# Kernel optimization log

Hardware: AMD Instinct MI355X
Metric: run time of the kernel (lower is better)

## Reference

```python
import jax, jax.numpy as jnp
import numpy as np

B, N, M, E, H, A = 2048, 768, 8192, 512, 8, 64  # batch, n, m, embed_dim, heads, head_dim(a)


def setup_inputs() -> dict:
    key = jax.random.key(0)
    ks = jax.random.split(key, 16)
    s = 0.02
    return {
        "x": jax.random.normal(ks[0], (B, N), jnp.float32),
        "X_cross": jax.random.normal(ks[1], (M, N), jnp.float32),
        # manual projection weights (used as x @ W, i.e. nn.Linear .weight of shape [out,in] -> here stored [n, E] etc.)
        "W_q_w": jax.random.normal(ks[2], (N, E), jnp.float32) * s,
        "W_k_w": jax.random.normal(ks[3], (N, E), jnp.float32) * s,
        "W_v_w": jax.random.normal(ks[4], (N, N), jnp.float32) * s,
        # nn.MultiheadAttention internal projections (vdim=n -> separate q/k/v weights)
        "q_w": jax.random.normal(ks[5], (E, E), jnp.float32) * s,
        "k_w": jax.random.normal(ks[6], (E, E), jnp.float32) * s,
        "v_w": jax.random.normal(ks[7], (E, N), jnp.float32) * s,
        "b_q": jax.random.normal(ks[8], (E,), jnp.float32) * s,
        "b_k": jax.random.normal(ks[9], (E,), jnp.float32) * s,
        "b_v": jax.random.normal(ks[10], (E,), jnp.float32) * s,
        "out_w": jax.random.normal(ks[11], (E, E), jnp.float32) * s,
        "out_b": jax.random.normal(ks[12], (E,), jnp.float32) * s,
        # final W_o: nn.Linear(E, n)
        "W_o_w": jax.random.normal(ks[13], (N, E), jnp.float32) * s,
        "W_o_b": jax.random.normal(ks[14], (N,), jnp.float32) * s,
    }


def reference(x, X_cross, W_q_w, W_k_w, W_v_w, q_w, k_w, v_w, b_q, b_k, b_v, out_w, out_b, W_o_w, W_o_b):
    inv_sqrt_a = jnp.float32(1.0 / np.sqrt(A))
    # manual projections (note: the F.layer_norm loop in the source is a no-op)
    Q = (x @ W_q_w) * inv_sqrt_a           # [B, E]; extra 1/sqrt(a) scaling applied pre-MHA
    K = X_cross @ W_k_w                    # [m, E]
    V = X_cross @ W_v_w                    # [m, n]
    # nn.MultiheadAttention (unbatched 2D inputs -> seq lens B and m)
    q = (Q @ q_w.T + b_q).reshape(B, H, A)
    k = (K @ k_w.T + b_k).reshape(M, H, A)
    v = (V @ v_w.T + b_v).reshape(M, H, A)
    scores = jnp.einsum('bha,mha->hbm', q, k) * inv_sqrt_a  # MHA's own 1/sqrt(head_dim)
    attn = jax.nn.softmax(scores, axis=-1)                  # [H, B, m]
    f = attn.mean(axis=0)                                   # averaged attn weights [B, m]
    ctx = jnp.einsum('hbm,mha->bha', attn, v).reshape(B, E)
    attn_out = ctx @ out_w.T + out_b                        # MHA out_proj -> [B, E]
    x_hat = attn_out @ W_o_w.T + W_o_b                      # [B, n]
    return (x, x_hat, f, V)
```

## Files before the change

### kernel.cpp

```cpp
#include <hip/hip_runtime.h>
#include <hip/hip_bf16.h>

typedef unsigned short u16;
typedef unsigned int u32;
typedef __attribute__((ext_vector_type(8))) __bf16 bf16x8;
typedef __attribute__((ext_vector_type(4))) float f32x4;

#define Bd  2048
#define Nd  768
#define Md  8192
#define Ed  512
#define Hd  8
#define NSL 8
#define AIT 16

__device__ __forceinline__ u16 f2bf(float f){
    union { __bf16 b; u16 u; } c; c.b = (__bf16)f; return c.u;
}
__device__ __forceinline__ float bf2f(u16 u){
    union { unsigned u; float f; } a; a.u = ((unsigned)u)<<16; return a.f;
}
__device__ __forceinline__ u32 pack2(float a, float b){
    union { ushort2 s; u32 u; } r;
    r.s.x = f2bf(a); r.s.y = f2bf(b);
    return r.u;
}
__device__ __forceinline__ float fexp2(float x){ return __builtin_amdgcn_exp2f(x); }

__device__ __forceinline__ void glds16(const void* g, void* l){
    __builtin_amdgcn_global_load_lds((const __attribute__((address_space(1))) void*)g,
                                     (__attribute__((address_space(3))) void*)l, 16, 0, 0);
}

struct CvtSeg { const float* src; u16* dst; float* dstf; int n4; };
struct PrepArgs {
    CvtSeg s[9]; int total4;
    const float* Wv; u16* WvT;
    const float* ow; u16* owT;
    const float* Wo; const float* ob; const float* Wob; float* bo;
    float* sume;
};
#define PREP_CVT_BLKS 10320
#define TCVT0_BLKS 576
#define TCVT1_BLKS 256
#define GEMV_BLKS 192
#define ZERO_BLKS 16

__global__ __launch_bounds__(256, 8)
void prep_k(PrepArgs a){
    __shared__ float t[32][33];
    const int bid = blockIdx.x, tid = threadIdx.x;
    if (bid < PREP_CVT_BLKS){
        int i = bid*256 + tid;
        if (i >= a.total4) return;
        #pragma unroll
        for (int k=0;k<9;k++){
            if (i < a.s[k].n4){
                float4 v = *(const float4*)(a.s[k].src + (size_t)i*4);
                if (a.s[k].dstf) *(float4*)(a.s[k].dstf + (size_t)i*4) = v;
                ushort4 u; u.x=f2bf(v.x); u.y=f2bf(v.y); u.z=f2bf(v.z); u.w=f2bf(v.w);
                *(ushort4*)(a.s[k].dst + (size_t)i*4) = u;
                return;
            }
            i -= a.s[k].n4;
        }
        return;
    }
    int local = bid - PREP_CVT_BLKS;
    if (local < TCVT0_BLKS + TCVT1_BLKS){
        const float* in; u16* out; int R, bx, by;
        if (local < TCVT0_BLKS){ in=a.Wv; out=a.WvT; R=Nd; bx=local%24; by=local/24; }
        else { int l2=local-TCVT0_BLKS; in=a.ow; out=a.owT; R=Ed; bx=l2%16; by=l2/16; }
        const int tx = tid & 31, ty = tid >> 5;
        const int r0 = by*32, c0 = bx*32;
        #pragma unroll
        for (int i=0;i<4;i++)
            t[ty + i*8][tx] = in[(size_t)(r0+ty+i*8)*R + c0+tx];
        __syncthreads();
        #pragma unroll
        for (int i=0;i<4;i++)
            out[(size_t)(c0+ty+i*8)*R + r0+tx] = f2bf(t[tx][ty+i*8]);
        return;
    }
    local -= TCVT0_BLKS + TCVT1_BLKS;
    if (local < GEMV_BLKS){
        const int wave = tid >> 6, lane = tid & 63;
        const int i = local*4 + wave;
        float s = 0.f;
        for (int j = lane; j < 512; j += 64) s += a.Wo[(size_t)i*512 + j] * a.ob[j];
        #pragma unroll
        for (int off = 32; off; off >>= 1) s += __shfl_down(s, off);
        if (lane == 0) a.bo[i] = s + a.Wob[i];
        return;
    }
    local -= GEMV_BLKS;
    {
        int idx = local*1024 + tid*4;
        *(float4*)(a.sume + idx) = make_float4(0.f,0.f,0.f,0.f);
    }
}

struct GSeg {
    const u16* A; const u16* B; void* C; const float* bias;
    int M, N, K; float alpha, bscale; int biasmode, outf32, blk0, nbx;
};
struct GBatch { GSeg s[5]; int nseg; };

__global__ __launch_bounds__(256, 3)
void gemm_multi(GBatch gb)
{
    __shared__ u16 lA[128*64];
    __shared__ u16 lB[128*64];
    const int bid = blockIdx.x;
    int si = 0;
    #pragma unroll
    for (int k=1;k<5;k++) if (k < gb.nseg && bid >= gb.s[k].blk0) si = k;
    const GSeg sg = gb.s[si];
    const int local = bid - sg.blk0;
    const int bx = local % sg.nbx, by = local / sg.nbx;
    const int K = sg.K, N = sg.N;

    const int tid = threadIdx.x;
    const int wave = tid >> 6, lane = tid & 63;
    const int wr = wave >> 1, wc = wave & 1;
    const size_t row0 = (size_t)by * 128;
    const size_t col0 = (size_t)bx * 128;

    f32x4 acc[4][4] = {};

    const int srow = wave*32 + (lane>>3);
    const int scol = (lane&7)*8;
    const u16* gA = sg.A + (row0 + srow)*(size_t)K + scol;
    const u16* gB = sg.B + (col0 + srow)*(size_t)K + scol;

    for (int kt = 0; kt < K; kt += 64) {
        #pragma unroll
        for (int i = 0; i < 4; ++i) {
            glds16(gA + (size_t)i*8*K + kt, lA + (wave*32 + i*8)*64);
            glds16(gB + (size_t)i*8*K + kt, lB + (wave*32 + i*8)*64);
        }
        __syncthreads();
        #pragma unroll
        for (int ks = 0; ks < 2; ++ks) {
            bf16x8 af[4], bfv[4];
            #pragma unroll
            for (int i = 0; i < 4; ++i)
                af[i] = *(const bf16x8*)&lA[(wr*64 + i*16 + (lane&15))*64 + ks*32 + (lane>>4)*8];
            #pragma unroll
            for (int i = 0; i < 4; ++i)
                bfv[i] = *(const bf16x8*)&lB[(wc*64 + i*16 + (lane&15))*64 + ks*32 + (lane>>4)*8];
            #pragma unroll
            for (int mi = 0; mi < 4; ++mi)
                #pragma unroll
                for (int ni = 0; ni < 4; ++ni)
                    acc[mi][ni] = __builtin_amdgcn_mfma_f32_16x16x32_bf16(af[mi], bfv[ni], acc[mi][ni], 0, 0, 0);
        }
        __syncthreads();
    }

    #pragma unroll
    for (int mi = 0; mi < 4; ++mi) {
        #pragma unroll
        for (int j = 0; j < 4; ++j) {
            const size_t r = row0 + wr*64 + mi*16 + (lane>>4)*4 + j;
            float badd_r = (sg.biasmode==2) ? sg.bias[r]*sg.bscale : 0.f;
            #pragma unroll
            for (int ni = 0; ni < 4; ++ni) {
                const size_t c = col0 + wc*64 + ni*16 + (lane&15);
                float bv = (sg.biasmode==1) ? sg.bias[c]*sg.bscale : badd_r;
                float v = acc[mi][ni][j] * sg.alpha + bv;
                if (sg.outf32) ((float*)sg.C)[r*(size_t)N + c] = v;
                else           ((u16*)sg.C)[r*(size_t)N + c] = f2bf(v);
            }
        }
    }
}

__global__ __launch_bounds__(256, 2)
void attn_sc(const u16* __restrict__ qp, const u16* __restrict__ kp,
             const u16* __restrict__ vTp, float* __restrict__ sumexp,
             u16* __restrict__ part)
{
    __shared__ u16 lK[2][64*64];
    __shared__ u16 lV[2][64*64];
    __shared__ u16 lP[4][64*64];
    const int tid = threadIdx.x, w = tid>>6, l = tid&63;
    const int g = l>>4, b15 = l&15;
    const int h = blockIdx.x & 7;
    const int rest = blockIdx.x >> 3;
    const int msl = rest & (NSL-1), bt = rest >> 3;
    const int m0 = msl * (AIT*64);

    bf16x8 qf[4][2];
    #pragma unroll
    for (int rt=0; rt<4; ++rt)
        #pragma unroll
        for (int ks=0; ks<2; ++ks)
            qf[rt][ks] = *(const bf16x8*)&qp[(size_t)(bt*256 + w*64 + rt*16 + b15)*512
                                            + h*64 + ks*32 + g*8];

    int addrW[4][4], addrR[4][2];
    #pragma unroll
    for (int rt=0; rt<4; ++rt){
        int bl = rt*16 + b15;
        #pragma unroll
        for (int ct=0; ct<4; ++ct){
            int chunk = ct*2 + (g>>1);
            addrW[rt][ct] = bl*128 + ((chunk ^ (bl&7))<<4) + (g&1)*8;
        }
        #pragma unroll
        for (int ks2=0; ks2<2; ++ks2)
            addrR[rt][ks2] = bl*128 + (((ks2*4+g) ^ (bl&7))<<4);
    }

    const int srcc = ((l&7) ^ (l>>3))*8;
    char* lPw = (char*)lP[w];

    auto STAGE = [&](int buf, int mb){
        #pragma unroll
        for (int i=0;i<2;i++)
            glds16(kp + (size_t)(mb + w*16 + i*8 + (l>>3))*512 + h*64 + srcc,
                   &lK[buf][(w*16 + i*8)*64]);
        #pragma unroll
        for (int i=0;i<2;i++)
            glds16(vTp + (size_t)(h*64 + w*16 + i*8 + (l>>3))*8192 + mb + srcc,
                   &lV[buf][(w*16 + i*8)*64]);
    };

    STAGE(0, m0);
    __syncthreads();

    f32x4 cacc[4][4] = {};
    float rs[4] = {};
    int cur = 0;
    for (int t=0; t<AIT; ++t){
        if (t+1 < AIT) STAGE(cur^1, m0 + (t+1)*64);

        f32x4 sacc[4][4] = {};
        #pragma unroll
        for (int ks=0; ks<2; ++ks){
            bf16x8 bk[4];
            #pragma unroll
            for (int ct=0; ct<4; ++ct)
                bk[ct] = *(const bf16x8*)&lK[cur][(ct*16+b15)*64 + (((ks*4+g) ^ (b15&7))<<3)];
            #pragma unroll
            for (int rt=0; rt<4; ++rt)
                #pragma unroll
                for (int ct=0; ct<4; ++ct)
                    sacc[rt][ct] = __builtin_amdgcn_mfma_f32_16x16x32_bf16(bk[ct], qf[rt][ks], sacc[rt][ct],0,0,0);
        }
        #pragma unroll
        for (int rt=0; rt<4; ++rt)
            #pragma unroll
            for (int ct=0; ct<4; ++ct){
                float p0 = fexp2(sacc[rt][ct][0]);
                float p1 = fexp2(sacc[rt][ct][1]);
                float p2 = fexp2(sacc[rt][ct][2]);
                float p3 = fexp2(sacc[rt][ct][3]);
                rs[rt] += (p0+p1)+(p2+p3);
                uint2 pk; pk.x = pack2(p0,p1); pk.y = pack2(p2,p3);
                *(uint2*)(lPw + addrW[rt][ct]) = pk;
            }
        #pragma unroll
        for (int ks2=0; ks2<2; ++ks2){
            bf16x8 vb[4];
            #pragma unroll
            for (int ai=0; ai<4; ++ai)
                vb[ai] = *(const bf16x8*)&lV[cur][(ai*16+b15)*64 + (((ks2*4+g) ^ (b15&7))<<3)];
            #pragma unroll
            for (int rt=0; rt<4; ++rt){
                bf16x8 pa = *(const bf16x8*)(lPw + addrR[rt][ks2]);
                #pragma unroll
                for (int ai=0; ai<4; ++ai)
                    cacc[rt][ai] = __builtin_amdgcn_mfma_f32_16x16x32_bf16(pa, vb[ai], cacc[rt][ai],0,0,0);
            }
        }
        __syncthreads();
        cur ^= 1;
    }

    #pragma unroll
    for (int rt=0; rt<4; ++rt)
        #pragma unroll
        for (int ai=0; ai<4; ++ai)
            #pragma unroll
            for (int j=0; j<4; ++j){
                size_t r = (size_t)bt*256 + w*64 + rt*16 + g*4 + j;
                size_t c = (size_t)h*64 + ai*16 + b15;
                part[((size_t)msl<<20) + r*512 + c] = f2bf(cacc[rt][ai][j]);
            }
    #pragma unroll
    for (int rt=0; rt<4; ++rt){
        float s = rs[rt];
        s += __shfl_xor(s, 16); s += __shfl_xor(s, 32);
        if (l < 16)
            atomicAdd(&sumexp[h*2048 + bt*256 + w*64 + rt*16 + l], s);
    }
}

__global__ void ctx_reduce_k(const u16* __restrict__ part, const float* __restrict__ sume,
                             u16* __restrict__ ctx){
    int i = (blockIdx.x*256 + threadIdx.x)*4;
    int b = i >> 9, h = (i >> 6) & 7;
    float ri = 1.0f / sume[h*2048 + b];
    float s0=0.f, s1=0.f, s2=0.f, s3=0.f;
    #pragma unroll
    for (int k=0;k<NSL;k++){
        ushort4 v = *(const ushort4*)(part + ((size_t)k<<20) + i);
        s0 += bf2f(v.x); s1 += bf2f(v.y); s2 += bf2f(v.z); s3 += bf2f(v.w);
    }
    ushort4 u;
    u.x = f2bf(s0*ri); u.y = f2bf(s1*ri); u.z = f2bf(s2*ri); u.w = f2bf(s3*ri);
    *(ushort4*)(ctx + i) = u;
}

struct FinArgs {
    const u16* ctxb; const u16* Woo2T; const float* bo; float* out_xhat;
    const u16* qp; const u16* kp; const float* sume; float* fo;
};
#define EPB 96

__global__ __launch_bounds__(256, 3)
void fin_k(FinArgs fa)
{
    __shared__ char smem[32768];
    const int tid = threadIdx.x;

    if (blockIdx.x < EPB){
        u16* lA = (u16*)smem;
        u16* lB = (u16*)(smem + 16384);
        const int local = blockIdx.x;
        const int bx = local % 6, by = local / 6;
        const int K = Ed, N = Nd;
        const int wave = tid >> 6, lane = tid & 63;
        const int wr = wave >> 1, wc = wave & 1;
        const size_t row0 = (size_t)by * 128;
        const size_t col0 = (size_t)bx * 128;
        f32x4 acc[4][4] = {};
        const int srow = wave*32 + (lane>>3);
        const int scol = (lane&7)*8;
        const u16* gA = fa.ctxb + (row0 + srow)*(size_t)K + scol;
        const u16* gB = fa.Woo2T + (col0 + srow)*(size_t)K + scol;
        for (int kt = 0; kt < K; kt += 64) {
            #pragma unroll
            for (int i = 0; i < 4; ++i) {
                glds16(gA + (size_t)i*8*K + kt, lA + (wave*32 + i*8)*64);
                glds16(gB + (size_t)i*8*K + kt, lB + (wave*32 + i*8)*64);
            }
            __syncthreads();
            #pragma unroll
            for (int ks = 0; ks < 2; ++ks) {
                bf16x8 af[4], bfv[4];
                #pragma unroll
                for (int i = 0; i < 4; ++i)
                    af[i] = *(const bf16x8*)&lA[(wr*64 + i*16 + (lane&15))*64 + ks*32 + (lane>>4)*8];
                #pragma unroll
                for (int i = 0; i < 4; ++i)
                    bfv[i] = *(const bf16x8*)&lB[(wc*64 + i*16 + (lane&15))*64 + ks*32 + (lane>>4)*8];
                #pragma unroll
                for (int mi = 0; mi < 4; ++mi)
                    #pragma unroll
                    for (int ni = 0; ni < 4; ++ni)
                        acc[mi][ni] = __builtin_amdgcn_mfma_f32_16x16x32_bf16(af[mi], bfv[ni], acc[mi][ni], 0, 0, 0);
            }
            __syncthreads();
        }
        #pragma unroll
        for (int mi = 0; mi < 4; ++mi)
            #pragma unroll
            for (int j = 0; j < 4; ++j) {
                const size_t r = row0 + wr*64 + mi*16 + (lane>>4)*4 + j;
                #pragma unroll
                for (int ni = 0; ni < 4; ++ni) {
                    const size_t c = col0 + wc*64 + ni*16 + (lane&15);
                    fa.out_xhat[r*(size_t)N + c] = acc[mi][ni][j] + fa.bo[c];
                }
            }
        return;
    }

    u16* lK0 = (u16*)smem;
    float* lR = (float*)(smem + 16384);
    const int w = tid>>6, l = tid&63;
    const int g = l>>4, b15 = l&15;
    const int bid = blockIdx.x - EPB;
    const int xcd = bid & 7, r2 = bid >> 3;
    const int mt = xcd*16 + (r2 & 15), bt = r2 >> 4;

    #pragma unroll
    for (int i=0;i<8;i++){
        int id = i*256 + tid;
        lR[id] = 0.125f / fa.sume[(id>>8)*2048 + bt*256 + (id&255)];
    }

    const int srcc = ((l&7) ^ (l>>3))*8;
    auto STAGE = [&](int buf, int h){
        #pragma unroll
        for (int i=0;i<2;i++)
            glds16(fa.kp + (size_t)(mt*64 + w*16 + i*8 + (l>>3))*512 + h*64 + srcc,
                   lK0 + buf*4096 + (w*16 + i*8)*64);
    };
    STAGE(0, 0);
    __syncthreads();

    f32x4 facc[4][4] = {};
    int cur = 0;
    for (int h=0; h<8; ++h){
        if (h<7) STAGE(cur^1, h+1);
        bf16x8 qf[4][2];
        #pragma unroll
        for (int rt=0; rt<4; ++rt)
            #pragma unroll
            for (int ks=0; ks<2; ++ks)
                qf[rt][ks] = *(const bf16x8*)&fa.qp[(size_t)(bt*256 + w*64 + rt*16 + b15)*512
                                                    + h*64 + ks*32 + g*8];
        #pragma unroll
        for (int ch=0; ch<2; ++ch){
            f32x4 sacc[4][2] = {};
            #pragma unroll
            for (int ks=0; ks<2; ++ks){
                bf16x8 bk[2];
                #pragma unroll
                for (int c2=0; c2<2; ++c2){
                    int ct = ch*2 + c2;
                    bk[c2] = *(const bf16x8*)&lK0[cur*4096 + (ct*16+b15)*64 + (((ks*4+g) ^ (b15&7))<<3)];
                }
                #pragma unroll
                for (int rt=0; rt<4; ++rt)
                    #pragma unroll
                    for (int c2=0; c2<2; ++c2)
                        sacc[rt][c2] = __builtin_amdgcn_mfma_f32_16x16x32_bf16(bk[c2], qf[rt][ks], sacc[rt][c2],0,0,0);
            }
            #pragma unroll
            for (int rt=0; rt<4; ++rt){
                float ri = lR[h*256 + w*64 + rt*16 + b15];
                #pragma unroll
                for (int c2=0; c2<2; ++c2)
                    #pragma unroll
                    for (int j=0;j<4;j++)
                        facc[rt][ch*2+c2][j] += fexp2(sacc[rt][c2][j]) * ri;
            }
        }
        __syncthreads();
        cur ^= 1;
    }
    #pragma unroll
    for (int rt=0; rt<4; ++rt){
        size_t b = (size_t)bt*256 + w*64 + rt*16 + b15;
        #pragma unroll
        for (int ct=0; ct<4; ++ct)
            *(float4*)&fa.fo[b*8192 + mt*64 + ct*16 + g*4] = *(float4*)&facc[rt][ct];
    }
}

extern "C" void kernel_launch(void* const* d_in, const int* in_sizes, int n_in,
                              void* d_out, int out_size, void* d_ws, size_t ws_size,
                              hipStream_t stream)
{
    const float* x   = (const float*)d_in[0];
    const float* Xc  = (const float*)d_in[1];
    const float* Wq  = (const float*)d_in[2];
    const float* Wk  = (const float*)d_in[3];
    const float* Wv  = (const float*)d_in[4];
    const float* qw  = (const float*)d_in[5];
    const float* kw  = (const float*)d_in[6];
    const float* vw  = (const float*)d_in[7];
    const float* bq  = (const float*)d_in[8];
    const float* bk  = (const float*)d_in[9];
    const float* bv  = (const float*)d_in[10];
    const float* ow  = (const float*)d_in[11];
    const float* ob  = (const float*)d_in[12];
    const float* Wo  = (const float*)d_in[13];
    const float* Wob = (const float*)d_in[14];

    float* out_x    = (float*)d_out;
    float* out_xhat = out_x + (size_t)Bd*Nd;
    float* out_f    = out_xhat + (size_t)Bd*Nd;
    float* out_V    = out_f + (size_t)Bd*Md;

    char* wsb = (char*)d_ws;
    size_t off = 0;
    auto alloc = [&](size_t bytes) -> void* {
        void* p = wsb + off; off += (bytes + 255) & ~(size_t)255; return p;
    };
    u16* xb     = (u16*)alloc((size_t)Bd*Nd*2);
    u16* Xb     = (u16*)alloc((size_t)Md*Nd*2);
    u16* qwb    = (u16*)alloc((size_t)Ed*Ed*2);
    u16* kwb    = (u16*)alloc((size_t)Ed*Ed*2);
    u16* vwb    = (u16*)alloc((size_t)Ed*Nd*2);
    u16* Wqb    = (u16*)alloc((size_t)Nd*Ed*2);
    u16* Wkb    = (u16*)alloc((size_t)Nd*Ed*2);
    u16* Wvb    = (u16*)alloc((size_t)Nd*Nd*2);
    u16* WvTb   = (u16*)alloc((size_t)Nd*Nd*2);
    u16* Wo_b   = (u16*)alloc((size_t)Nd*Ed*2);
    u16* owTb   = (u16*)alloc((size_t)Ed*Ed*2);
    u16* WqqT   = (u16*)alloc((size_t)Ed*Nd*2);
    u16* WkkT   = (u16*)alloc((size_t)Ed*Nd*2);
    u16* WvvT   = (u16*)alloc((size_t)Ed*Nd*2);
    u16* Woo2T  = (u16*)alloc((size_t)Nd*Ed*2);
    float* bo   = (float*)alloc((size_t)Nd*4);
    u16* qb     = (u16*)alloc((size_t)Bd*Ed*2);
    u16* kb     = (u16*)alloc((size_t)Md*Ed*2);
    u16* vTb    = (u16*)alloc((size_t)Ed*Md*2);
    u16* ctxb   = (u16*)alloc((size_t)Bd*Ed*2);
    float* sume = (float*)alloc((size_t)Hd*Bd*4);
    u16* part   = (u16*)alloc((size_t)NSL*Bd*Ed*2);
    if (off > ws_size) return;

    const float LOG2E = 1.44269504f;

    PrepArgs pa;
    pa.s[0] = { x,  xb,  out_x,   Bd*Nd/4 };
    pa.s[1] = { Xc, Xb,  nullptr, Md*Nd/4 };
    pa.s[2] = { qw, qwb, nullptr, Ed*Ed/4 };
    pa.s[3] = { kw, kwb, nullptr, Ed*Ed/4 };
    pa.s[4] = { vw, vwb, nullptr, Ed*Nd/4 };
    pa.s[5] = { Wq, Wqb, nullptr, Nd*Ed/4 };
    pa.s[6] = { Wk, Wkb, nullptr, Nd*Ed/4 };
    pa.s[7] = { Wv, Wvb, nullptr, Nd*Nd/4 };
    pa.s[8] = { Wo, Wo_b, nullptr, Nd*Ed/4 };
    pa.total4 = (Bd*Nd + Md*Nd + Ed*Ed*2 + Ed*Nd + Nd*Ed*2 + Nd*Nd + Nd*Ed)/4;
    pa.Wv = Wv; pa.WvT = WvTb; pa.ow = ow; pa.owT = owTb;
    pa.Wo = Wo; pa.ob = ob; pa.Wob = Wob; pa.bo = bo;
    pa.sume = sume;
    prep_k<<<PREP_CVT_BLKS + TCVT0_BLKS + TCVT1_BLKS + GEMV_BLKS + ZERO_BLKS, 256, 0, stream>>>(pa);

    {
        GBatch gb; gb.nseg = 5;
        gb.s[0] = { qwb, Wqb, WqqT, nullptr, Ed, Nd, Ed, 0.125f*0.125f*LOG2E, 1.f, 0, 0,   0, Nd/128 };
        gb.s[1] = { kwb, Wkb, WkkT, nullptr, Ed, Nd, Ed, 1.f, 1.f, 0, 0,  24, Nd/128 };
        gb.s[2] = { vwb, Wvb, WvvT, nullptr, Ed, Nd, Nd, 1.f, 1.f, 0, 0,  48, Nd/128 };
        gb.s[3] = { Wo_b, owTb, Woo2T, nullptr, Nd, Ed, Ed, 1.f, 1.f, 0, 0,  72, Ed/128 };
        gb.s[4] = { Xb, WvTb, out_V, nullptr, Md, Nd, Nd, 1.f, 1.f, 0, 1,  96, Nd/128 };
        gemm_multi<<<96 + (Md/128)*(Nd/128), 256, 0, stream>>>(gb);
    }
    {
        GBatch gb; gb.nseg = 3;
        gb.s[0] = { xb, WqqT, qb, bq, Bd, Ed, Nd, 1.f, 0.125f*LOG2E, 1, 0,   0, Ed/128 };
        gb.s[1] = { Xb, WkkT, kb, bk, Md, Ed, Nd, 1.f, 1.f, 1, 0,  64, Ed/128 };
        gb.s[2] = { WvvT, Xb, vTb, bv, Ed, Md, Nd, 1.f, 1.f, 2, 0, 320, Md/128 };
        gb.s[3] = gb.s[0]; gb.s[4] = gb.s[0];
        gemm_multi<<<320 + (Ed/128)*(Md/128), 256, 0, stream>>>(gb);
    }

    attn_sc<<<512, 256, 0, stream>>>(qb, kb, vTb, sume, part);
    ctx_reduce_k<<<Bd*Ed/1024, 256, 0, stream>>>(part, sume, ctxb);
    FinArgs fa = { ctxb, Woo2T, bo, out_xhat, qb, kb, sume, out_f };
    fin_k<<<EPB + 1024, 256, 0, stream>>>(fa);
}
```

Measured before the change: 179.2 us.

## Stage full K tile for all heads in LDS and prefetch Q fragments

The attention-weights part of the final kernel now loads the whole 64x512 K tile covering all eight heads into LDS once, with an XOR swizzle, instead of double-buffering one head at a time with a barrier per head. Q fragments for the next head are prefetched into registers while the current head computes. The head loop is fully unrolled and computes all four column tiles per pass, and the x_hat GEMM blocks move to the end of the grid. This removes per-head barriers and staging but raises LDS use to 72KB and lowers the occupancy target to 2 blocks per SM, so latency hiding may suffer.

```diff
diff --git a/kernel.cpp b/kernel.cpp
--- a/kernel.cpp
+++ b/kernel.cpp
@@ -318,18 +318,18 @@
     const u16* ctxb; const u16* Woo2T; const float* bo; float* out_xhat;
     const u16* qp; const u16* kp; const float* sume; float* fo;
 };
-#define EPB 96
-
-__global__ __launch_bounds__(256, 3)
+#define AFB 1024
+
+__global__ __launch_bounds__(256, 2)
 void fin_k(FinArgs fa)
 {
-    __shared__ char smem[32768];
+    __shared__ char smem[73728];
     const int tid = threadIdx.x;
 
-    if (blockIdx.x < EPB){
+    if (blockIdx.x >= AFB){
         u16* lA = (u16*)smem;
         u16* lB = (u16*)(smem + 16384);
-        const int local = blockIdx.x;
+        const int local = blockIdx.x - AFB;
         const int bx = local % 6, by = local / 6;
         const int K = Ed, N = Nd;
         const int wave = tid >> 6, lane = tid & 63;
@@ -379,11 +379,11 @@
         return;
     }
 
-    u16* lK0 = (u16*)smem;
-    float* lR = (float*)(smem + 16384);
+    u16* lK = (u16*)smem;
+    float* lR = (float*)(smem + 65536);
     const int w = tid>>6, l = tid&63;
     const int g = l>>4, b15 = l&15;
-    const int bid = blockIdx.x - EPB;
+    const int bid = blockIdx.x;
     const int xcd = bid & 7, r2 = bid >> 3;
     const int mt = xcd*16 + (r2 & 15), bt = r2 >> 4;
 
@@ -392,57 +392,61 @@
         int id = i*256 + tid;
         lR[id] = 0.125f / fa.sume[(id>>8)*2048 + bt*256 + (id&255)];
     }
-
-    const int srcc = ((l&7) ^ (l>>3))*8;
-    auto STAGE = [&](int buf, int h){
-        #pragma unroll
-        for (int i=0;i<2;i++)
-            glds16(fa.kp + (size_t)(mt*64 + w*16 + i*8 + (l>>3))*512 + h*64 + srcc,
-                   lK0 + buf*4096 + (w*16 + i*8)*64);
-    };
-    STAGE(0, 0);
+    #pragma unroll
+    for (int i=0;i<16;i++){
+        int row = w*16 + i;
+        int sc = (l & 56) | ((l ^ row) & 7);
+        glds16(fa.kp + (size_t)(mt*64 + row)*512 + sc*8, lK + row*512);
+    }
     __syncthreads();
 
     f32x4 facc[4][4] = {};
-    int cur = 0;
+    bf16x8 qfA[4][2], qfB[4][2];
+    const u16* qbase = fa.qp + (size_t)(bt*256 + w*64 + b15)*512 + g*8;
+    #pragma unroll
+    for (int rt=0; rt<4; ++rt)
+        #pragma unroll
+        for (int ks=0; ks<2; ++ks)
+            qfA[rt][ks] = *(const bf16x8*)&qbase[(size_t)(rt*16)*512 + ks*32];
+
+    #pragma unroll
     for (int h=0; h<8; ++h){
-        if (h<7) STAGE(cur^1, h+1);
-        bf16x8 qf[4][2];
-        #pragma unroll
-        for (int rt=0; rt<4; ++rt)
-            #pragma unroll
-            for (int ks=0; ks<2; ++ks)
-                qf[rt][ks] = *(const bf16x8*)&fa.qp[(size_t)(bt*256 + w*64 + rt*16 + b15)*512
-                                                    + h*64 + ks*32 + g*8];
-        #pragma unroll
-        for (int ch=0; ch<2; ++ch){
-            f32x4 sacc[4][2] = {};
-            #pragma unroll
-            for (int ks=0; ks<2; ++ks){
-                bf16x8 bk[2];
-                #pragma unroll
-                for (int c2=0; c2<2; ++c2){
-                    int ct = ch*2 + c2;
-                    bk[c2] = *(const bf16x8*)&lK0[cur*4096 + (ct*16+b15)*64 + (((ks*4+g) ^ (b15&7))<<3)];
+        if (h < 7){
+            #pragma unroll
+            for (int rt=0; rt<4; ++rt)
+                #pragma unroll
+                for (int ks=0; ks<2; ++ks){
+                    bf16x8 v = *(const bf16x8*)&qbase[(size_t)(rt*16)*512 + (h+1)*64 + ks*32];
+                    if (h&1) qfA[rt][ks] = v; else qfB[rt][ks] = v;
                 }
-                #pragma unroll
-                for (int rt=0; rt<4; ++rt)
-                    #pragma unroll
-                    for (int c2=0; c2<2; ++c2)
-                        sacc[rt][c2] = __builtin_amdgcn_mfma_f32_16x16x32_bf16(bk[c2], qf[rt][ks], sacc[rt][c2],0,0,0);
+        }
+        f32x4 sacc[4][4] = {};
+        #pragma unroll
+        for (int ks=0; ks<2; ++ks){
+            bf16x8 bk[4];
+            #pragma unroll
+            for (int ct=0; ct<4; ++ct){
+                int rb = ct*16 + b15;
+                int chunk = h*8 + (((ks*4+g) ^ (rb&7)));
+                bk[ct] = *(const bf16x8*)&lK[rb*512 + chunk*8];
             }
             #pragma unroll
             for (int rt=0; rt<4; ++rt){
-                float ri = lR[h*256 + w*64 + rt*16 + b15];
-                #pragma unroll
-                for (int c2=0; c2<2; ++c2)
-                    #pragma unroll
-                    for (int j=0;j<4;j++)
-                        facc[rt][ch*2+c2][j] += fexp2(sacc[rt][c2][j]) * ri;
-            }
-        }
-        __syncthreads();
-        cur ^= 1;
+                bf16x8 qv = (h&1) ? qfB[rt][ks] : qfA[rt][ks];
+                #pragma unroll
+                for (int ct=0; ct<4; ++ct)
+                    sacc[rt][ct] = __builtin_amdgcn_mfma_f32_16x16x32_bf16(bk[ct], qv, sacc[rt][ct],0,0,0);
+            }
+        }
+        #pragma unroll
+        for (int rt=0; rt<4; ++rt){
+            float ri = lR[h*256 + w*64 + rt*16 + b15];
+            #pragma unroll
+            for (int ct=0; ct<4; ++ct)
+                #pragma unroll
+                for (int j=0;j<4;j++)
+                    facc[rt][ct][j] += fexp2(sacc[rt][ct][j]) * ri;
+        }
     }
     #pragma unroll
     for (int rt=0; rt<4; ++rt){
@@ -546,5 +550,5 @@
     attn_sc<<<512, 256, 0, stream>>>(qb, kb, vTb, sume, part);
     ctx_reduce_k<<<Bd*Ed/1024, 256, 0, stream>>>(part, sume, ctxb);
     FinArgs fa = { ctxb, Woo2T, bo, out_xhat, qb, kb, sume, out_f };
-    fin_k<<<EPB + 1024, 256, 0, stream>>>(fa);
-}
+    fin_k<<<AFB + 96, 256, 0, stream>>>(fa);
+}
```

New measurement: 334.5 us. 86.7% more time.
